# Performance work log

Hardware: AMD Instinct MI355X
Metric: run time of the kernel (lower is better)

The kernel has to match this reference:

```python
import jax, jax.numpy as jnp
import numpy as np

K = 24       # conv feature channels
D = 8        # spatial grid side
QST = 11
OUT = 28
HID = 256
PAIR_FEAT = 2 * (K + 2) + QST  # 63


def _linear(x, w, b):
    return x @ w + b


def setup_inputs() -> dict:
    key = jax.random.key(0)
    ks = jax.random.split(key, 16)
    b = 64
    def w(k, fan_in, fan_out):
        return jax.random.normal(k, (fan_in, fan_out), jnp.float32) / np.sqrt(fan_in)
    inp = {
        "x": jax.random.normal(ks[0], (b, K, D, D), jnp.float32),
        "qst": jax.random.normal(ks[1], (b, QST), jnp.float32),
        "g1_w": w(ks[2], PAIR_FEAT, HID), "g1_b": jnp.zeros((HID,), jnp.float32),
        "g2_w": w(ks[3], HID, HID),       "g2_b": jnp.zeros((HID,), jnp.float32),
        "g3_w": w(ks[4], HID, HID),       "g3_b": jnp.zeros((HID,), jnp.float32),
        "g4_w": w(ks[5], HID, HID),       "g4_b": jnp.zeros((HID,), jnp.float32),
        "f1_w": w(ks[6], HID, HID),       "f1_b": jnp.zeros((HID,), jnp.float32),
        "f2_w": w(ks[7], HID, HID),       "f2_b": jnp.zeros((HID,), jnp.float32),
        "f3_w": w(ks[8], HID, OUT),       "f3_b": jnp.zeros((OUT,), jnp.float32),
    }
    return inp


def reference(x, qst, g1_w, g1_b, g2_w, g2_b, g3_w, g3_b, g4_w, g4_b,
              f1_w, f1_b, f2_w, f2_b, f3_w, f3_b):
    b, k, d, _ = x.shape
    d2 = d * d
    # coordinate channels: x-coord varies along columns, y-coord along rows
    coords = jnp.linspace(-d / 2.0, d / 2.0, d, dtype=x.dtype)
    cx = jnp.broadcast_to(coords[None, :], (d, d))   # x-coordinate
    cy = jnp.broadcast_to(coords[:, None], (d, d))   # y-coordinate
    ct = jnp.broadcast_to(jnp.stack([cx, cy])[None], (b, 2, d, d))
    x_coords = jnp.concatenate([x, ct], axis=1)            # (b, k+2, d, d)
    o = x_coords.reshape(b, k + 2, d2).transpose(0, 2, 1)  # (b, d2, k+2) objects

    # pair features: [o_q, o_p, qst] matching torch x_full[b,p,q] = [x_i=o[q], x_j=(o[p],qst)]
    f_i = jnp.broadcast_to(o[:, None, :, :], (b, d2, d2, k + 2))
    f_j = jnp.broadcast_to(o[:, :, None, :], (b, d2, d2, k + 2))
    f_q = jnp.broadcast_to(qst[:, None, None, :], (b, d2, d2, qst.shape[1]))
    pairs = jnp.concatenate([f_i, f_j, f_q], axis=-1).reshape(b * d2 * d2, -1)

    h = jax.nn.relu(_linear(pairs, g1_w, g1_b))
    h = jax.nn.relu(_linear(h, g2_w, g2_b))
    h = jax.nn.relu(_linear(h, g3_w, g3_b))
    h = jax.nn.relu(_linear(h, g4_w, g4_b))
    x_g = h.reshape(b, d2 * d2, HID).sum(axis=1)  # sum over all d^4 pairs

    x_f = jax.nn.relu(_linear(x_g, f1_w, f1_b))
    x_f = jax.nn.relu(_linear(x_f, f2_w, f2_b))  # dropout is identity in eval
    x_f = _linear(x_f, f3_w, f3_b)
    return jax.nn.log_softmax(x_f, axis=1)
```

## Files before the change

kernel.cpp:

```cpp
#include <hip/hip_runtime.h>
#include <hip/hip_bf16.h>
#include <math.h>

#define NB   64
#define D2   64
#define OBJ  26
#define NQST 11
#define HID  256
#define NOUT 28
#define NTILE 32
#define HSTRE 264

typedef _Float16 f16x8 __attribute__((ext_vector_type(8)));
typedef _Float16 f16x4 __attribute__((ext_vector_type(4)));
typedef __attribute__((ext_vector_type(4))) float f32x4;
typedef __attribute__((ext_vector_type(2))) unsigned int u32x2;

__device__ __forceinline__ unsigned pack_h2(float a, float b) {
    auto r = __builtin_amdgcn_cvt_pkrtz(a, b);
    union U { decltype(r) h; unsigned u; } v;
    v.h = r;
    return v.u;
}
__device__ __forceinline__ f16x8 relu8(f16x8 x) {
    f16x8 z = {0, 0, 0, 0, 0, 0, 0, 0};
#if __has_builtin(__builtin_elementwise_max)
    return __builtin_elementwise_max(x, z);
#else
    #pragma unroll
    for (int j = 0; j < 8; ++j) x[j] = x[j] > (_Float16)0 ? x[j] : (_Float16)0;
    return x;
#endif
}
__device__ __forceinline__ u32x2 pack_relu4(float a0, float a1, float a2, float a3) {
    u32x2 w;
    w[0] = pack_h2(a0, a1);
    w[1] = pack_h2(a2, a3);
#if __has_builtin(__builtin_elementwise_max)
    union { u32x2 u; f16x4 h; } v;
    v.u = w;
    f16x4 z = {0, 0, 0, 0};
    v.h = __builtin_elementwise_max(v.h, z);
    return v.u;
#else
    union { u32x2 u; f16x4 h; } v; v.u = w;
    #pragma unroll
    for (int j = 0; j < 4; ++j) v.h[j] = v.h[j] > (_Float16)0 ? v.h[j] : (_Float16)0;
    return v.u;
#endif
}

__global__ __launch_bounds__(256) void prep_all(
        const float* __restrict__ x, const float* __restrict__ qst,
        const float* __restrict__ g1_w, const float* __restrict__ g1_b,
        const float* __restrict__ g2_w, const float* __restrict__ g3_w,
        const float* __restrict__ g4_w,
        _Float16* __restrict__ Abf, _Float16* __restrict__ Bbf,
        _Float16* __restrict__ Wt) {
    if (blockIdx.x < 384) {
        int blk = blockIdx.x;
        int ks = blk & 7;
        int nbl = blk >> 3;
        int l = nbl >> 4;
        int nb = nbl & 15;
        const float* W = (l == 0) ? g2_w : ((l == 1) ? g3_w : g4_w);
        int t = threadIdx.x;
        #pragma unroll
        for (int u = 0; u < 2; ++u) {
            int e = t + u * 256;
            int lane = e >> 3;
            int j = e & 7;
            int n = nb * 16 + (lane & 15);
            int k = ks * 32 + (lane >> 4) * 8 + j;
            Wt[blk * 512 + e] = (_Float16)W[k * HID + n];
        }
        return;
    }
    int blk = blockIdx.x - 384;
    int b = blk >> 2;
    int q0 = (blk & 3) * 16;
    int tid = threadIdx.x;
    __shared__ float o_lds[16][OBJ];
    for (int idx = tid; idx < 24 * 16; idx += 256) {
        int c = idx >> 4, i = idx & 15;
        o_lds[i][c] = x[(b * 24 + c) * D2 + q0 + i];
    }
    if (tid < 16) {
        int q = q0 + tid;
        o_lds[tid][24] = (float)(q & 7) * (8.0f / 7.0f) - 4.0f;
        o_lds[tid][25] = (float)(q >> 3) * (8.0f / 7.0f) - 4.0f;
    }
    __syncthreads();
    int n = tid;
    float qpart = g1_b[n];
    for (int s = 0; s < NQST; ++s)
        qpart += qst[b * NQST + s] * g1_w[(2 * OBJ + s) * HID + n];
    float accA[16], accB[16];
    #pragma unroll
    for (int i = 0; i < 16; ++i) { accA[i] = 0.f; accB[i] = 0.f; }
    for (int c = 0; c < OBJ; ++c) {
        float wA = g1_w[c * HID + n];
        float wB = g1_w[(OBJ + c) * HID + n];
        #pragma unroll
        for (int i = 0; i < 16; ++i) {
            float ov = o_lds[i][c];
            accA[i] += ov * wA;
            accB[i] += ov * wB;
        }
    }
    #pragma unroll
    for (int i = 0; i < 16; ++i) {
        int q = q0 + i;
        Abf[(b * D2 + q) * HID + n] = (_Float16)accA[i];
        Bbf[(b * D2 + q) * HID + n] = (_Float16)(accB[i] + qpart);
    }
}


__device__ __forceinline__ void stage_h(
        _Float16* hbuf, const _Float16* __restrict__ Ab,
        const _Float16* __restrict__ Bb, int tid) {
    #pragma unroll 2
    for (int i = 0; i < 8; ++i) {
        int c = tid + i * 256;
        int m = c >> 5;
        int k0 = (c & 31) * 8;
        f16x8 av = *(const f16x8*)(Ab + m * HID + k0);
        f16x8 bv = *(const f16x8*)(Bb + k0);
        f16x8 hv = relu8(av + bv);
        *(f16x8*)(hbuf + m * HSTRE + k0) = hv;
    }
}

__device__ __forceinline__ void layer_sw(
        const _Float16* __restrict__ Wl, const float* __restrict__ bias,
        const _Float16* hin, _Float16* hout,
        int wid, int rg, int col, int lane) {
    const _Float16* wb0 = Wl + (size_t)(wid * 4 + 0) * 4096 + lane * 8;
    const _Float16* wb1 = Wl + (size_t)(wid * 4 + 1) * 4096 + lane * 8;
    const _Float16* wb2 = Wl + (size_t)(wid * 4 + 2) * 4096 + lane * 8;
    const _Float16* wb3 = Wl + (size_t)(wid * 4 + 3) * 4096 + lane * 8;

    f32x4 acc[4][4];
    #pragma unroll
    for (int nf = 0; nf < 4; ++nf) {
        f32x4 b4 = *(const f32x4*)(bias + wid * 64 + nf * 16 + rg * 4);
        #pragma unroll
        for (int mf = 0; mf < 4; ++mf)
            acc[nf][mf] = b4;
    }

    const _Float16* hr0 = hin + (0 * 16 + col) * HSTRE + rg * 8;
    const _Float16* hr1 = hin + (1 * 16 + col) * HSTRE + rg * 8;
    const _Float16* hr2 = hin + (2 * 16 + col) * HSTRE + rg * 8;
    const _Float16* hr3 = hin + (3 * 16 + col) * HSTRE + rg * 8;

    f16x8 wbuf[2][4];
    wbuf[0][0] = *(const f16x8*)(wb0);
    wbuf[0][1] = *(const f16x8*)(wb1);
    wbuf[0][2] = *(const f16x8*)(wb2);
    wbuf[0][3] = *(const f16x8*)(wb3);

    #pragma unroll
    for (int ks = 0; ks < 8; ++ks) {
        const int cur = ks & 1;
        if (ks < 7) {
            int off = (ks + 1) * 512;
            wbuf[cur ^ 1][0] = *(const f16x8*)(wb0 + off);
            wbuf[cur ^ 1][1] = *(const f16x8*)(wb1 + off);
            wbuf[cur ^ 1][2] = *(const f16x8*)(wb2 + off);
            wbuf[cur ^ 1][3] = *(const f16x8*)(wb3 + off);
        }
        f16x8 hfr[4];
        hfr[0] = *(const f16x8*)(hr0 + ks * 32);
        hfr[1] = *(const f16x8*)(hr1 + ks * 32);
        hfr[2] = *(const f16x8*)(hr2 + ks * 32);
        hfr[3] = *(const f16x8*)(hr3 + ks * 32);
        __builtin_amdgcn_s_setprio(1);
        #pragma unroll
        for (int nf = 0; nf < 4; ++nf)
            #pragma unroll
            for (int mf = 0; mf < 4; ++mf)
                acc[nf][mf] = __builtin_amdgcn_mfma_f32_16x16x32_f16(
                    wbuf[cur][nf], hfr[mf], acc[nf][mf], 0, 0, 0);
        __builtin_amdgcn_s_setprio(0);
    }
    #pragma unroll
    for (int nf = 0; nf < 4; ++nf) {
        int n0 = wid * 64 + nf * 16 + rg * 4;
        #pragma unroll
        for (int mf = 0; mf < 4; ++mf) {
            int m = mf * 16 + col;
            u32x2 w = pack_relu4(acc[nf][mf][0], acc[nf][mf][1],
                                 acc[nf][mf][2], acc[nf][mf][3]);
            *(u32x2*)(hout + m * HSTRE + n0) = w;
        }
    }
}

__device__ __forceinline__ void layer2_red(
        const _Float16* __restrict__ Wl, const float* __restrict__ bias,
        const _Float16* hin, float* pacc, int wid, int rg, int col, int lane) {
    const _Float16* wb0 = Wl + (size_t)(wid * 4 + 0) * 4096 + lane * 8;
    const _Float16* wb1 = Wl + (size_t)(wid * 4 + 1) * 4096 + lane * 8;
    const _Float16* wb2 = Wl + (size_t)(wid * 4 + 2) * 4096 + lane * 8;
    const _Float16* wb3 = Wl + (size_t)(wid * 4 + 3) * 4096 + lane * 8;

    f32x4 acc[4][4];
    #pragma unroll
    for (int nf = 0; nf < 4; ++nf) {
        float bv = bias[wid * 64 + nf * 16 + col];
        f32x4 bb = (f32x4){bv, bv, bv, bv};
        #pragma unroll
        for (int mf = 0; mf < 4; ++mf)
            acc[mf][nf] = bb;
    }

    const _Float16* hr0 = hin + (0 * 16 + col) * HSTRE + rg * 8;
    const _Float16* hr1 = hin + (1 * 16 + col) * HSTRE + rg * 8;
    const _Float16* hr2 = hin + (2 * 16 + col) * HSTRE + rg * 8;
    const _Float16* hr3 = hin + (3 * 16 + col) * HSTRE + rg * 8;

    f16x8 wbuf[2][4];
    wbuf[0][0] = *(const f16x8*)(wb0);
    wbuf[0][1] = *(const f16x8*)(wb1);
    wbuf[0][2] = *(const f16x8*)(wb2);
    wbuf[0][3] = *(const f16x8*)(wb3);

    #pragma unroll
    for (int ks = 0; ks < 8; ++ks) {
        const int cur = ks & 1;
        if (ks < 7) {
            int off = (ks + 1) * 512;
            wbuf[cur ^ 1][0] = *(const f16x8*)(wb0 + off);
            wbuf[cur ^ 1][1] = *(const f16x8*)(wb1 + off);
            wbuf[cur ^ 1][2] = *(const f16x8*)(wb2 + off);
            wbuf[cur ^ 1][3] = *(const f16x8*)(wb3 + off);
        }
        f16x8 hfr[4];
        hfr[0] = *(const f16x8*)(hr0 + ks * 32);
        hfr[1] = *(const f16x8*)(hr1 + ks * 32);
        hfr[2] = *(const f16x8*)(hr2 + ks * 32);
        hfr[3] = *(const f16x8*)(hr3 + ks * 32);
        __builtin_amdgcn_s_setprio(1);
        #pragma unroll
        for (int mf = 0; mf < 4; ++mf)
            #pragma unroll
            for (int nf = 0; nf < 4; ++nf)
                acc[mf][nf] = __builtin_amdgcn_mfma_f32_16x16x32_f16(
                    hfr[mf], wbuf[cur][nf], acc[mf][nf], 0, 0, 0);
        __builtin_amdgcn_s_setprio(0);
    }
    #pragma unroll
    for (int nf = 0; nf < 4; ++nf) {
        float s = 0.f;
        #pragma unroll
        for (int mf = 0; mf < 4; ++mf)
            #pragma unroll
            for (int r = 0; r < 4; ++r)
                s += fmaxf(acc[mf][nf][r], 0.f);
        s += __shfl_xor(s, 16);
        s += __shfl_xor(s, 32);
        pacc[nf] += s;
    }
}

__global__ __launch_bounds__(256, 2) void rn_main(
        const _Float16* __restrict__ Abf, const _Float16* __restrict__ Bbf,
        const _Float16* __restrict__ Wt,
        const float* __restrict__ g2_b, const float* __restrict__ g3_b,
        const float* __restrict__ g4_b, float* __restrict__ partial) {
    int wg = blockIdx.x;
    int swz = (wg & 7) * 256 + (wg >> 3);
    int b = swz >> 5;
    int t = swz & 31;

    __shared__ _Float16 h0[D2 * HSTRE];
    __shared__ _Float16 h1[D2 * HSTRE];

    int tid = threadIdx.x;
    int lane = tid & 63;
    int wid = tid >> 6;
    int rg = lane >> 4;
    int col = lane & 15;

    const _Float16* Ab  = Abf + (size_t)(b * D2) * HID;
    const _Float16* Bb0 = Bbf + (size_t)(b * D2 + t * 2 + 0) * HID;
    const _Float16* Bb1 = Bbf + (size_t)(b * D2 + t * 2 + 1) * HID;
    const _Float16* W0 = Wt;
    const _Float16* W1 = Wt + (size_t)1 * 65536;
    const _Float16* W2 = Wt + (size_t)2 * 65536;

    float pacc[4] = {0.f, 0.f, 0.f, 0.f};

    stage_h(h0, Ab, Bb0, tid);
    __syncthreads();
    layer_sw(W0, g2_b, h0, h1, wid, rg, col, lane);
    __syncthreads();
    layer_sw(W1, g3_b, h1, h0, wid, rg, col, lane);
    __syncthreads();
    layer2_red(W2, g4_b, h0, pacc, wid, rg, col, lane);
    stage_h(h1, Ab, Bb1, tid);
    __syncthreads();

    layer_sw(W0, g2_b, h1, h0, wid, rg, col, lane);
    __syncthreads();
    layer_sw(W1, g3_b, h0, h1, wid, rg, col, lane);
    __syncthreads();
    layer2_red(W2, g4_b, h1, pacc, wid, rg, col, lane);

    if (rg == 0) {
        #pragma unroll
        for (int nf = 0; nf < 4; ++nf)
            partial[(size_t)(b * NTILE + t) * HID + wid * 64 + nf * 16 + col]
                = pacc[nf];
    }
}

__global__ __launch_bounds__(1024) void fuse_kernel(
        const float* __restrict__ partial,
        const float* __restrict__ f1_w, const float* __restrict__ f1_b,
        const float* __restrict__ f2_w, const float* __restrict__ f2_b,
        const float* __restrict__ f3_w, const float* __restrict__ f3_b,
        float* __restrict__ out) {
    int b = blockIdx.x;
    int tid = threadIdx.x;
    int n = tid & 255;
    int kg = tid >> 8;
    __shared__ float xg[HID];
    __shared__ float pbuf[4][HID];
    __shared__ float h1[HID];
    __shared__ float h2v[HID];
    __shared__ float lred[NOUT];
    __shared__ float lse;

    {
        float s = 0.f;
        #pragma unroll
        for (int u = 0; u < 8; ++u)
            s += partial[(size_t)(b * NTILE + kg * 8 + u) * HID + n];
        pbuf[kg][n] = s;
    }
    __syncthreads();
    if (tid < HID)
        xg[n] = pbuf[0][n] + pbuf[1][n] + pbuf[2][n] + pbuf[3][n];
    __syncthreads();

    {
        float a = 0.f;
        #pragma unroll 4
        for (int k = kg * 64; k < kg * 64 + 64; ++k)
            a += xg[k] * f1_w[k * HID + n];
        pbuf[kg][n] = a;
    }
    __syncthreads();
    if (tid < HID) {
        float a1 = f1_b[n] + pbuf[0][n] + pbuf[1][n] + pbuf[2][n] + pbuf[3][n];
        h1[n] = a1 > 0.f ? a1 : 0.f;
    }
    __syncthreads();

    {
        float a = 0.f;
        #pragma unroll 4
        for (int k = kg * 64; k < kg * 64 + 64; ++k)
            a += h1[k] * f2_w[k * HID + n];
        pbuf[kg][n] = a;
    }
    __syncthreads();
    if (tid < HID) {
        float a2 = f2_b[n] + pbuf[0][n] + pbuf[1][n] + pbuf[2][n] + pbuf[3][n];
        h2v[n] = a2 > 0.f ? a2 : 0.f;
    }
    __syncthreads();

    if (n < NOUT) {
        float a = 0.f;
        #pragma unroll 4
        for (int k = kg * 64; k < kg * 64 + 64; ++k)
            a += h2v[k] * f3_w[k * NOUT + n];
        pbuf[kg][n] = a;
    }
    __syncthreads();
    if (tid < NOUT)
        lred[tid] = f3_b[tid] + pbuf[0][tid] + pbuf[1][tid]
                  + pbuf[2][tid] + pbuf[3][tid];
    __syncthreads();
    if (tid == 0) {
        float mx = lred[0];
        for (int j = 1; j < NOUT; ++j) mx = fmaxf(mx, lred[j]);
        float se = 0.f;
        for (int j = 0; j < NOUT; ++j) se += expf(lred[j] - mx);
        lse = mx + logf(se);
    }
    __syncthreads();
    if (tid < NOUT)
        out[b * NOUT + tid] = lred[tid] - lse;
}

extern "C" void kernel_launch(void* const* d_in, const int* in_sizes, int n_in,
                              void* d_out, int out_size, void* d_ws, size_t ws_size,
                              hipStream_t stream) {
    const float* x    = (const float*)d_in[0];
    const float* qst  = (const float*)d_in[1];
    const float* g1_w = (const float*)d_in[2];
    const float* g1_b = (const float*)d_in[3];
    const float* g2_w = (const float*)d_in[4];
    const float* g2_b = (const float*)d_in[5];
    const float* g3_w = (const float*)d_in[6];
    const float* g3_b = (const float*)d_in[7];
    const float* g4_w = (const float*)d_in[8];
    const float* g4_b = (const float*)d_in[9];
    const float* f1_w = (const float*)d_in[10];
    const float* f1_b = (const float*)d_in[11];
    const float* f2_w = (const float*)d_in[12];
    const float* f2_b = (const float*)d_in[13];
    const float* f3_w = (const float*)d_in[14];
    const float* f3_b = (const float*)d_in[15];
    float* out = (float*)d_out;

    char* ws = (char*)d_ws;
    _Float16* Abf = (_Float16*)ws;
    _Float16* Bbf = (_Float16*)(ws + (2u << 20));
    _Float16* Wt  = (_Float16*)(ws + (4u << 20));
    float* partial = (float*)(ws + (4u << 20) + (512u << 10));

    prep_all<<<384 + 4 * NB, 256, 0, stream>>>(x, qst, g1_w, g1_b, g2_w, g3_w, g4_w,
                                               Abf, Bbf, Wt);
    rn_main<<<NB * NTILE, 256, 0, stream>>>(Abf, Bbf, Wt, g2_b, g3_b, g4_b, partial);
    fuse_kernel<<<NB, 1024, 0, stream>>>(partial, f1_w, f1_b, f2_w, f2_b, f3_w, f3_b, out);
}
```

Before: 115.0 us.

## Use single in-place LDS buffer and drop weight double-buffering for 3 blocks/CU

Replaces the two ping-pong LDS activation buffers with one buffer updated in place, adding a barrier between the MFMA reads and the writeback in each hidden layer. It also removes register double-buffering of weight fragments and raises launch bounds from 2 to 3 blocks per CU. The aim is to halve LDS use and cut registers so more workgroups are resident to hide latency. In exchange, weight loads are no longer prefetched ahead of the MFMAs and each layer carries an extra barrier.

```diff
diff --git a/kernel.cpp b/kernel.cpp
--- a/kernel.cpp
+++ b/kernel.cpp
@@ -132,10 +132,9 @@
     }
 }
 
-__device__ __forceinline__ void layer_sw(
+__device__ __forceinline__ void layer_sw_ip(
         const _Float16* __restrict__ Wl, const float* __restrict__ bias,
-        const _Float16* hin, _Float16* hout,
-        int wid, int rg, int col, int lane) {
+        _Float16* h, int wid, int rg, int col, int lane) {
     const _Float16* wb0 = Wl + (size_t)(wid * 4 + 0) * 4096 + lane * 8;
     const _Float16* wb1 = Wl + (size_t)(wid * 4 + 1) * 4096 + lane * 8;
     const _Float16* wb2 = Wl + (size_t)(wid * 4 + 2) * 4096 + lane * 8;
@@ -150,27 +149,18 @@
             acc[nf][mf] = b4;
     }
 
-    const _Float16* hr0 = hin + (0 * 16 + col) * HSTRE + rg * 8;
-    const _Float16* hr1 = hin + (1 * 16 + col) * HSTRE + rg * 8;
-    const _Float16* hr2 = hin + (2 * 16 + col) * HSTRE + rg * 8;
-    const _Float16* hr3 = hin + (3 * 16 + col) * HSTRE + rg * 8;
-
-    f16x8 wbuf[2][4];
-    wbuf[0][0] = *(const f16x8*)(wb0);
-    wbuf[0][1] = *(const f16x8*)(wb1);
-    wbuf[0][2] = *(const f16x8*)(wb2);
-    wbuf[0][3] = *(const f16x8*)(wb3);
+    const _Float16* hr0 = h + (0 * 16 + col) * HSTRE + rg * 8;
+    const _Float16* hr1 = h + (1 * 16 + col) * HSTRE + rg * 8;
+    const _Float16* hr2 = h + (2 * 16 + col) * HSTRE + rg * 8;
+    const _Float16* hr3 = h + (3 * 16 + col) * HSTRE + rg * 8;
 
     #pragma unroll
     for (int ks = 0; ks < 8; ++ks) {
-        const int cur = ks & 1;
-        if (ks < 7) {
-            int off = (ks + 1) * 512;
-            wbuf[cur ^ 1][0] = *(const f16x8*)(wb0 + off);
-            wbuf[cur ^ 1][1] = *(const f16x8*)(wb1 + off);
-            wbuf[cur ^ 1][2] = *(const f16x8*)(wb2 + off);
-            wbuf[cur ^ 1][3] = *(const f16x8*)(wb3 + off);
-        }
+        f16x8 wfr[4];
+        wfr[0] = *(const f16x8*)(wb0 + ks * 512);
+        wfr[1] = *(const f16x8*)(wb1 + ks * 512);
+        wfr[2] = *(const f16x8*)(wb2 + ks * 512);
+        wfr[3] = *(const f16x8*)(wb3 + ks * 512);
         f16x8 hfr[4];
         hfr[0] = *(const f16x8*)(hr0 + ks * 32);
         hfr[1] = *(const f16x8*)(hr1 + ks * 32);
@@ -182,9 +172,10 @@
             #pragma unroll
             for (int mf = 0; mf < 4; ++mf)
                 acc[nf][mf] = __builtin_amdgcn_mfma_f32_16x16x32_f16(
-                    wbuf[cur][nf], hfr[mf], acc[nf][mf], 0, 0, 0);
+                    wfr[nf], hfr[mf], acc[nf][mf], 0, 0, 0);
         __builtin_amdgcn_s_setprio(0);
     }
+    __syncthreads();
     #pragma unroll
     for (int nf = 0; nf < 4; ++nf) {
         int n0 = wid * 64 + nf * 16 + rg * 4;
@@ -193,9 +184,10 @@
             int m = mf * 16 + col;
             u32x2 w = pack_relu4(acc[nf][mf][0], acc[nf][mf][1],
                                  acc[nf][mf][2], acc[nf][mf][3]);
-            *(u32x2*)(hout + m * HSTRE + n0) = w;
+            *(u32x2*)(h + m * HSTRE + n0) = w;
         }
     }
+    __syncthreads();
 }
 
 __device__ __forceinline__ void layer2_red(
@@ -221,22 +213,13 @@
     const _Float16* hr2 = hin + (2 * 16 + col) * HSTRE + rg * 8;
     const _Float16* hr3 = hin + (3 * 16 + col) * HSTRE + rg * 8;
 
-    f16x8 wbuf[2][4];
-    wbuf[0][0] = *(const f16x8*)(wb0);
-    wbuf[0][1] = *(const f16x8*)(wb1);
-    wbuf[0][2] = *(const f16x8*)(wb2);
-    wbuf[0][3] = *(const f16x8*)(wb3);
-
     #pragma unroll
     for (int ks = 0; ks < 8; ++ks) {
-        const int cur = ks & 1;
-        if (ks < 7) {
-            int off = (ks + 1) * 512;
-            wbuf[cur ^ 1][0] = *(const f16x8*)(wb0 + off);
-            wbuf[cur ^ 1][1] = *(const f16x8*)(wb1 + off);
-            wbuf[cur ^ 1][2] = *(const f16x8*)(wb2 + off);
-            wbuf[cur ^ 1][3] = *(const f16x8*)(wb3 + off);
-        }
+        f16x8 wfr[4];
+        wfr[0] = *(const f16x8*)(wb0 + ks * 512);
+        wfr[1] = *(const f16x8*)(wb1 + ks * 512);
+        wfr[2] = *(const f16x8*)(wb2 + ks * 512);
+        wfr[3] = *(const f16x8*)(wb3 + ks * 512);
         f16x8 hfr[4];
         hfr[0] = *(const f16x8*)(hr0 + ks * 32);
         hfr[1] = *(const f16x8*)(hr1 + ks * 32);
@@ -248,7 +231,7 @@
             #pragma unroll
             for (int nf = 0; nf < 4; ++nf)
                 acc[mf][nf] = __builtin_amdgcn_mfma_f32_16x16x32_f16(
-                    hfr[mf], wbuf[cur][nf], acc[mf][nf], 0, 0, 0);
+                    hfr[mf], wfr[nf], acc[mf][nf], 0, 0, 0);
         __builtin_amdgcn_s_setprio(0);
     }
     #pragma unroll
@@ -265,7 +248,7 @@
     }
 }
 
-__global__ __launch_bounds__(256, 2) void rn_main(
+__global__ __launch_bounds__(256, 3) void rn_main(
         const _Float16* __restrict__ Abf, const _Float16* __restrict__ Bbf,
         const _Float16* __restrict__ Wt,
         const float* __restrict__ g2_b, const float* __restrict__ g3_b,
@@ -275,8 +258,7 @@
     int b = swz >> 5;
     int t = swz & 31;
 
-    __shared__ _Float16 h0[D2 * HSTRE];
-    __shared__ _Float16 h1[D2 * HSTRE];
+    __shared__ _Float16 h[D2 * HSTRE];
 
     int tid = threadIdx.x;
     int lane = tid & 63;
@@ -293,21 +275,18 @@
 
     float pacc[4] = {0.f, 0.f, 0.f, 0.f};
 
-    stage_h(h0, Ab, Bb0, tid);
-    __syncthreads();
-    layer_sw(W0, g2_b, h0, h1, wid, rg, col, lane);
-    __syncthreads();
-    layer_sw(W1, g3_b, h1, h0, wid, rg, col, lane);
-    __syncthreads();
-    layer2_red(W2, g4_b, h0, pacc, wid, rg, col, lane);
-    stage_h(h1, Ab, Bb1, tid);
-    __syncthreads();
-
-    layer_sw(W0, g2_b, h1, h0, wid, rg, col, lane);
-    __syncthreads();
-    layer_sw(W1, g3_b, h0, h1, wid, rg, col, lane);
-    __syncthreads();
-    layer2_red(W2, g4_b, h1, pacc, wid, rg, col, lane);
+    stage_h(h, Ab, Bb0, tid);
+    __syncthreads();
+    layer_sw_ip(W0, g2_b, h, wid, rg, col, lane);
+    layer_sw_ip(W1, g3_b, h, wid, rg, col, lane);
+    layer2_red(W2, g4_b, h, pacc, wid, rg, col, lane);
+    __syncthreads();
+
+    stage_h(h, Ab, Bb1, tid);
+    __syncthreads();
+    layer_sw_ip(W0, g2_b, h, wid, rg, col, lane);
+    layer_sw_ip(W1, g3_b, h, wid, rg, col, lane);
+    layer2_red(W2, g4_b, h, pacc, wid, rg, col, lane);
 
     if (rg == 0) {
         #pragma unroll
```

After: 159.1 us. +38.3%, slower.
